# Kernel optimization log

Hardware: AMD Instinct MI355X
Metric: run time of the kernel (lower is better)

## Reference

```python
import jax, jax.numpy as jnp
import numpy as np

N, E, B = 50000, 800000, 64          # nodes, edges, graphs
D_IN, HID, OUT, HEADS = 128, 64, 32, 4
NEG_SLOPE, BN_EPS = 0.2, 1e-5


def gat_conv(x, src, dst, W, a_src, a_dst, bias):
    """PyG-style GATConv (concat heads). x:[n,din], W:[din,H*C], a_*:[H,C]."""
    n = x.shape[0]
    H, C = a_src.shape
    xl = (x @ W).reshape(n, H, C)                      # [n,H,C]
    e_s = jnp.einsum('nhc,hc->nh', xl, a_src)          # alpha_src per node
    e_d = jnp.einsum('nhc,hc->nh', xl, a_dst)          # alpha_dst per node
    e = jax.nn.leaky_relu(e_s[src] + e_d[dst], NEG_SLOPE)   # [E,H]
    m = jax.ops.segment_max(e, dst, num_segments=n)
    m = jnp.where(jnp.isfinite(m), m, 0.0)             # guard isolated nodes
    p = jnp.exp(e - m[dst])
    s = jax.ops.segment_sum(p, dst, num_segments=n)
    alpha = p / (s[dst] + 1e-16)                       # edge softmax over in-edges
    out = jax.ops.segment_sum(alpha[:, :, None] * xl[src], dst, num_segments=n)
    return out.reshape(n, H * C) + bias


def batch_norm(h, gamma, beta):
    mu = h.mean(0)
    var = h.var(0)
    return (h - mu) * jax.lax.rsqrt(var + BN_EPS) * gamma + beta


def setup_inputs() -> dict:
    key = jax.random.key(0)
    ks = jax.random.split(key, 18)
    sc = 0.05
    x = jax.random.normal(ks[0], (N, D_IN), jnp.float32)
    edge_index = jax.random.randint(ks[1], (2, E), 0, N, jnp.int32)
    batch = jnp.sort(jax.random.randint(ks[2], (N,), 0, B, jnp.int32))
    C1 = HID // HEADS
    return {
        'x': x, 'edge_index': edge_index, 'batch': batch,
        'W1': jax.random.normal(ks[3], (D_IN, HID), jnp.float32) * sc,
        'a_src1': jax.random.normal(ks[4], (HEADS, C1), jnp.float32) * sc,
        'a_dst1': jax.random.normal(ks[5], (HEADS, C1), jnp.float32) * sc,
        'b1': jnp.zeros((HID,), jnp.float32),
        'g1': jnp.ones((HID,), jnp.float32),
        'be1': jnp.zeros((HID,), jnp.float32),
        'W2': jax.random.normal(ks[6], (HID, OUT), jnp.float32) * sc,
        'a_src2': jax.random.normal(ks[7], (1, OUT), jnp.float32) * sc,
        'a_dst2': jax.random.normal(ks[8], (1, OUT), jnp.float32) * sc,
        'b2': jnp.zeros((OUT,), jnp.float32),
        'g2': jnp.ones((OUT,), jnp.float32),
        'be2': jnp.zeros((OUT,), jnp.float32),
        'fcW1': jax.random.normal(ks[9], (2 * OUT, OUT), jnp.float32) * sc,
        'fcb1': jnp.zeros((OUT,), jnp.float32),
        'fcW2': jax.random.normal(ks[10], (OUT, OUT), jnp.float32) * sc,
        'fcb2': jnp.zeros((OUT,), jnp.float32),
    }


def reference(x, edge_index, batch, W1, a_src1, a_dst1, b1, g1, be1,
              W2, a_src2, a_dst2, b2, g2, be2, fcW1, fcb1, fcW2, fcb2):
    n = x.shape[0]
    loops = jnp.arange(n, dtype=edge_index.dtype)
    src = jnp.concatenate([edge_index[0], loops])   # PyG add_self_loops
    dst = jnp.concatenate([edge_index[1], loops])

    h = gat_conv(x, src, dst, W1, a_src1, a_dst1, b1)
    h = jax.nn.relu(batch_norm(h, g1, be1))          # dropout: eval no-op
    h = gat_conv(h, src, dst, W2, a_src2, a_dst2, b2)
    node_emb = batch_norm(h, g2, be2)                # [N, OUT]

    cnt = jax.ops.segment_sum(jnp.ones((n,), node_emb.dtype), batch, num_segments=B)
    gmean = jax.ops.segment_sum(node_emb, batch, num_segments=B) / jnp.maximum(cnt, 1.0)[:, None]
    gmax = jax.ops.segment_max(node_emb, batch, num_segments=B)
    gmax = jnp.where(jnp.isfinite(gmax), gmax, 0.0)
    g = jnp.concatenate([gmean, gmax], axis=1)       # [B, 2*OUT]
    g = jax.nn.relu(g @ fcW1 + fcb1)
    graph_emb = g @ fcW2 + fcb2                      # [B, OUT]
    return node_emb, graph_emb
```

## Files before the change

kernel.cpp:

```cpp
#include <hip/hip_runtime.h>
#include <math.h>

#define N_NODES 50000
#define N_EDGES 800000
#define N_GRAPHS 64
#define D_IN 128
#define HID 64
#define OUT_C 32
#define NEG 0.2f
#define BN_EPS 1e-5f
#define N_TILES 3125
#define N_BUCKETS 196
#define BIN_CHUNK 4096
#define BIN_NB 196
#define GEMM1_NB 782
#define BUCKET_CAP 5120
#define PHANTOM N_NODES

typedef __attribute__((ext_vector_type(8))) short short8;
typedef __attribute__((ext_vector_type(4))) float f32x4;

static __device__ inline unsigned short f2bf(float f) {
    unsigned u = __float_as_uint(f);
    u += 0x7FFF + ((u >> 16) & 1);
    return (unsigned short)(u >> 16);
}
static __device__ inline float bfl(unsigned u) { return __uint_as_float(u << 16); }
static __device__ inline float bfh(unsigned u) { return __uint_as_float(u & 0xFFFF0000u); }


__global__ void __launch_bounds__(256) k_front(
        const int* __restrict__ src, const int* __restrict__ dst,
        int* __restrict__ gcur, unsigned* __restrict__ ebuf,
        const float* __restrict__ x, const float* __restrict__ W1,
        const float* __restrict__ a_src1, const float* __restrict__ a_dst1,
        unsigned short* __restrict__ xl1b, float* __restrict__ esd1,
        unsigned short* __restrict__ xl2b, float* __restrict__ esd2,
        const int* __restrict__ batch, int* __restrict__ gstart) {
    __shared__ __align__(16) char smem[23616];
    int tid = threadIdx.x;
    int blk = blockIdx.x;

    if (blk < BIN_NB) {
        int* cnt = (int*)smem;
        int* lofs = cnt + 256;
        int* dstoff = lofs + 256;
        int* ws4 = dstoff + 256;
        unsigned* stage = (unsigned*)(ws4 + 4);
        unsigned char* stage_b = (unsigned char*)(stage + BIN_CHUNK);
        cnt[tid] = 0;
        __syncthreads();
        int e0 = blk * BIN_CHUNK;
        int ne = N_EDGES - e0; if (ne > BIN_CHUNK) ne = BIN_CHUNK;
        unsigned rec[16]; int bkt[16], lp[16];
        #pragma unroll
        for (int j = 0; j < 16; ++j) {
            int r = j * 256 + tid;
            if (r < ne) {
                int e = e0 + r;
                int s = src[e], d = dst[e];
                rec[j] = ((unsigned)s << 8) | (unsigned)(d & 255);
                bkt[j] = d >> 8;
                lp[j] = atomicAdd(&cnt[bkt[j]], 1);
            } else bkt[j] = -1;
        }
        __syncthreads();
        int v = cnt[tid];
        int lane = tid & 63, wid = tid >> 6;
        int incl = v;
        #pragma unroll
        for (int off = 1; off < 64; off <<= 1) {
            int t = __shfl_up(incl, off, 64);
            if (lane >= off) incl += t;
        }
        if (lane == 63) ws4[wid] = incl;
        __syncthreads();
        if (tid == 0) {
            int a = ws4[0];
            #pragma unroll
            for (int j = 1; j < 4; ++j) { a += ws4[j]; ws4[j] = a; }
        }
        __syncthreads();
        if (wid > 0) incl += ws4[wid - 1];
        lofs[tid] = incl - v;
        __syncthreads();
        #pragma unroll
        for (int j = 0; j < 16; ++j) {
            if (bkt[j] >= 0) {
                int idx = lofs[bkt[j]] + lp[j];
                stage[idx] = rec[j];
                stage_b[idx] = (unsigned char)bkt[j];
            }
        }
        if (tid < N_BUCKETS && cnt[tid] > 0) {
            int g = atomicAdd(&gcur[tid], cnt[tid]);
            dstoff[tid] = tid * BUCKET_CAP + g - lofs[tid];
        }
        __syncthreads();
        for (int i = tid; i < ne; i += 256) {
            int b = stage_b[i];
            ebuf[dstoff[b] + i] = stage[i];
        }
        return;
    }

    if (blk < BIN_NB + GEMM1_NB) {
        typedef unsigned short WtRow[144];
        WtRow* Wt = (WtRow*)smem;
        for (int i = tid; i < 80 * 128; i += 256) {
            int n = i >> 7, k = i & 127;
            float v;
            if (n < 64) v = W1[k * 64 + n];
            else if (n < 72) {
                int hh = (n - 64) & 3;
                const float* a = ((n - 64) < 4 ? a_src1 : a_dst1) + hh * 16;
                v = 0.f;
                #pragma unroll
                for (int c = 0; c < 16; ++c) v = fmaf(W1[k * 64 + hh * 16 + c], a[c], v);
            } else v = 0.f;
            Wt[n][k] = f2bf(v);
        }
        __syncthreads();
        int lane = tid & 63, wid = tid >> 6;
        int tile = (blk - BIN_NB) * 4 + wid;
        if (tile >= N_TILES) return;
        int m = lane & 15, kg = lane >> 4;
        int base = tile * 16;
        const float* xr = x + (size_t)(base + m) * D_IN + kg * 8;
        f32x4 acc[5];
        #pragma unroll
        for (int t = 0; t < 5; ++t) acc[t] = (f32x4){0.f, 0.f, 0.f, 0.f};
        #pragma unroll
        for (int s = 0; s < 4; ++s) {
            f32x4 p = ((const f32x4*)(xr + s * 32))[0];
            f32x4 q = ((const f32x4*)(xr + s * 32))[1];
            short8 a;
            a[0] = (short)f2bf(p[0]); a[1] = (short)f2bf(p[1]);
            a[2] = (short)f2bf(p[2]); a[3] = (short)f2bf(p[3]);
            a[4] = (short)f2bf(q[0]); a[5] = (short)f2bf(q[1]);
            a[6] = (short)f2bf(q[2]); a[7] = (short)f2bf(q[3]);
            #pragma unroll
            for (int t = 0; t < 5; ++t) {
                short8 b = *(const short8*)&Wt[t * 16 + m][s * 32 + kg * 8];
                acc[t] = __builtin_amdgcn_mfma_f32_16x16x32_bf16(a, b, acc[t], 0, 0, 0);
            }
        }
        #pragma unroll
        for (int r = 0; r < 4; ++r) {
            int node = base + kg * 4 + r;
            #pragma unroll
            for (int t = 0; t < 4; ++t)
                xl1b[(size_t)node * HID + t * 16 + m] = f2bf(acc[t][r]);
            if (m < 8) esd1[node * 8 + m] = acc[4][r];
        }
        return;
    }

    if (tid <= N_GRAPHS) {
        int g = tid;
        int lo = 0, hi = N_NODES;
        while (lo < hi) {
            int mid = (lo + hi) >> 1;
            if (batch[mid] < g) lo = mid + 1; else hi = mid;
        }
        gstart[g] = lo;
    }
    if (tid >= 128 && tid < 192) xl1b[(size_t)PHANTOM * HID + (tid - 128)] = 0;
    if (tid >= 192 && tid < 200) esd1[(size_t)PHANTOM * 8 + (tid - 192)] = -1e30f;
    if (tid >= 200 && tid < 232) xl2b[(size_t)PHANTOM * OUT_C + (tid - 200)] = 0;
    if (tid >= 232 && tid < 234) esd2[(size_t)PHANTOM * 2 + (tid - 232)] = -1e30f;
}


__global__ void __launch_bounds__(256) k_countscan(
        const unsigned* __restrict__ ebuf, const int* __restrict__ gcur,
        int* __restrict__ counts, int* __restrict__ row_start,
        int* __restrict__ bsum) {
    __shared__ int lcnt[256];
    __shared__ int ws[4];
    int tid = threadIdx.x, b = blockIdx.x;
    lcnt[tid] = 0;
    __syncthreads();
    int ne = gcur[b];
    const unsigned* eb = ebuf + (size_t)b * BUCKET_CAP;
    for (int i = tid; i < ne; i += 256)
        atomicAdd(&lcnt[eb[i] & 255u], 1);
    __syncthreads();
    int node = b * 256 + tid;
    int raw = lcnt[tid];
    if (node < N_NODES) counts[node] = raw;
    int v = (node < N_NODES) ? ((raw + 3) & ~3) : 0;
    int lane = tid & 63, wid = tid >> 6;
    int incl = v;
    #pragma unroll
    for (int off = 1; off < 64; off <<= 1) {
        int t = __shfl_up(incl, off, 64);
        if (lane >= off) incl += t;
    }
    if (lane == 63) ws[wid] = incl;
    __syncthreads();
    if (tid == 0) {
        int a = ws[0];
        #pragma unroll
        for (int j = 1; j < 4; ++j) { a += ws[j]; ws[j] = a; }
    }
    __syncthreads();
    if (wid > 0) incl += ws[wid - 1];
    if (node < N_NODES) row_start[node + 1] = incl;
    if (tid == 255) bsum[b] = incl;
}


__global__ void __launch_bounds__(256) k_fillrs(
        const unsigned* __restrict__ ebuf, const int* __restrict__ gcur,
        const int* __restrict__ bsum, const int* __restrict__ counts,
        int* __restrict__ row_start, int* __restrict__ col) {
    __shared__ int lcur[256], rs[256];
    __shared__ int wsum4[4];
    __shared__ int btot;
    int tid = threadIdx.x, b = blockIdx.x;
    int lane = tid & 63, wid = tid >> 6;
    int v = (tid < b) ? bsum[tid] : 0;
    #pragma unroll
    for (int off = 32; off; off >>= 1) v += __shfl_down(v, off, 64);
    if (lane == 0) wsum4[wid] = v;
    __syncthreads();
    if (tid == 0) btot = wsum4[0] + wsum4[1] + wsum4[2] + wsum4[3];
    __syncthreads();
    int boffv = btot;
    int node = b * 256 + tid;
    int intra = (tid == 0) ? 0 : row_start[node];
    int rsf = boffv + intra;
    if (node < N_NODES) {
        row_start[node] = rsf;
        rs[tid] = rsf;
        if (node == N_NODES - 1)
            row_start[N_NODES] = rsf + ((counts[node] + 3) & ~3);
    } else rs[tid] = 0;
    lcur[tid] = 0;
    __syncthreads();
    int ne = gcur[b];
    const unsigned* eb = ebuf + (size_t)b * BUCKET_CAP;
    for (int i = tid; i < ne; i += 256) {
        unsigned e = eb[i];
        int li = e & 255u;
        int p = atomicAdd(&lcur[li], 1);
        col[rs[li] + p] = (int)(e >> 8);
    }
    if (node < N_NODES) {
        int cnt = counts[node];
        int pe = (cnt + 3) & ~3;
        for (int j = cnt; j < pe; ++j) col[rsf + j] = PHANTOM;
    }
}


__global__ void __launch_bounds__(256) k_agg1(
        const unsigned* __restrict__ xl1r, const float* __restrict__ esd1,
        const int* __restrict__ row_start, const int* __restrict__ col,
        const float* __restrict__ b1, float* __restrict__ h1pre) {
    int wid = threadIdx.x >> 6, lane = threadIdx.x & 63;
    int d = blockIdx.x * 4 + wid;
    if (d >= N_NODES) return;
    int c2 = lane & 31, half = lane >> 5;
    int h = c2 >> 3;
    float edh = esd1[d * 8 + 4 + h];
    float ax = 0.f, ay = 0.f, wsum = 0.f;
    if (half == 0) {
        float e0 = esd1[d * 8 + h] + edh;
        float w0 = __expf(fmaxf(e0, NEG * e0));
        unsigned u = xl1r[(size_t)d * 32 + c2];
        ax = w0 * bfl(u); ay = w0 * bfh(u); wsum = w0;
    }
    int js = row_start[d], je = row_start[d + 1];
    for (int j0 = js; j0 < je; j0 += 64) {
        int sv = col[j0 + lane];
        int cnt = je - j0; if (cnt > 64) cnt = 64;
        for (int k = 0; k < cnt; k += 4) {
            int sa = __shfl(sv, k + half, 64);
            int sb = __shfl(sv, k + 2 + half, 64);
            unsigned ua = xl1r[(size_t)sa * 32 + c2];
            unsigned ub = xl1r[(size_t)sb * 32 + c2];
            float ea = esd1[sa * 8 + h] + edh;
            float eb = esd1[sb * 8 + h] + edh;
            float wa = __expf(fmaxf(ea, NEG * ea));
            float wb = __expf(fmaxf(eb, NEG * eb));
            ax = fmaf(wa, bfl(ua), ax); ay = fmaf(wa, bfh(ua), ay);
            ax = fmaf(wb, bfl(ub), ax); ay = fmaf(wb, bfh(ub), ay);
            wsum += wa + wb;
        }
    }
    ax += __shfl_xor(ax, 32, 64);
    ay += __shfl_xor(ay, 32, 64);
    wsum += __shfl_xor(wsum, 32, 64);
    if (half == 0) {
        float2 bb = ((const float2*)b1)[c2];
        float inv = 1.f / wsum;
        float2 r;
        r.x = ax * inv + bb.x;
        r.y = ay * inv + bb.y;
        ((float2*)h1pre)[(size_t)d * 32 + c2] = r;
    }
}


__global__ void __launch_bounds__(256) k_stats(const float* __restrict__ hpre,
                                               int nch, float* __restrict__ stats) {
    int c = threadIdx.x & (nch - 1);
    int gid = blockIdx.x * blockDim.x + threadIdx.x;
    int r0 = gid / nch;
    int rstride = (gridDim.x * blockDim.x) / nch;
    float s = 0.f, s2 = 0.f;
    for (int n = r0; n < N_NODES; n += rstride) {
        float v = hpre[(size_t)n * nch + c];
        s += v;
        s2 = fmaf(v, v, s2);
    }
    __shared__ float ls[256], ls2[256];
    ls[threadIdx.x] = s;
    ls2[threadIdx.x] = s2;
    __syncthreads();
    if (threadIdx.x < nch) {
        int rows = 256 / nch;
        float a = 0.f, b = 0.f;
        for (int r = 0; r < rows; ++r) {
            a += ls[r * nch + c];
            b += ls2[r * nch + c];
        }
        atomicAdd(&stats[c], a);
        atomicAdd(&stats[nch + c], b);
    }
}


__global__ void __launch_bounds__(256) k_gemm2(
        const float* __restrict__ h1pre, const float* __restrict__ stats1,
        const float* __restrict__ g1, const float* __restrict__ be1,
        const float* __restrict__ W2, const float* __restrict__ a_src2,
        const float* __restrict__ a_dst2,
        unsigned short* __restrict__ xl2b, float* __restrict__ esd2) {
    __shared__ unsigned short Wt[48][80];
    __shared__ float A1s[64], B1s[64];
    int tid = threadIdx.x;
    for (int i = tid; i < 48 * 64; i += 256) {
        int n = i >> 6, k = i & 63;
        float v;
        if (n < 32) v = W2[k * 32 + n];
        else if (n < 34) {
            const float* a = (n == 32) ? a_src2 : a_dst2;
            v = 0.f;
            #pragma unroll
            for (int c = 0; c < 32; ++c) v = fmaf(W2[k * 32 + c], a[c], v);
        } else v = 0.f;
        Wt[n][k] = f2bf(v);
    }
    if (tid < 64) {
        float mu = stats1[tid] * (1.f / N_NODES);
        float var = stats1[64 + tid] * (1.f / N_NODES) - mu * mu;
        float sc = g1[tid] * rsqrtf(var + BN_EPS);
        A1s[tid] = sc;
        B1s[tid] = be1[tid] - mu * sc;
    }
    __syncthreads();
    int lane = tid & 63, wid = tid >> 6;
    int tile = blockIdx.x * 4 + wid;
    if (tile >= N_TILES) return;
    int m = lane & 15, kg = lane >> 4;
    int base = tile * 16;
    const float* hr = h1pre + (size_t)(base + m) * HID + kg * 8;
    f32x4 acc[3];
    #pragma unroll
    for (int t = 0; t < 3; ++t) acc[t] = (f32x4){0.f, 0.f, 0.f, 0.f};
    #pragma unroll
    for (int s = 0; s < 2; ++s) {
        int k0 = s * 32 + kg * 8;
        f32x4 p = ((const f32x4*)(hr + s * 32))[0];
        f32x4 q = ((const f32x4*)(hr + s * 32))[1];
        f32x4 sa = *(const f32x4*)&A1s[k0];
        f32x4 sb = *(const f32x4*)&B1s[k0];
        f32x4 sa2 = *(const f32x4*)&A1s[k0 + 4];
        f32x4 sb2 = *(const f32x4*)&B1s[k0 + 4];
        short8 a;
        #pragma unroll
        for (int j = 0; j < 4; ++j) {
            float v = fmaf(p[j], sa[j], sb[j]);
            a[j] = (short)f2bf(v > 0.f ? v : 0.f);
        }
        #pragma unroll
        for (int j = 0; j < 4; ++j) {
            float v = fmaf(q[j], sa2[j], sb2[j]);
            a[4 + j] = (short)f2bf(v > 0.f ? v : 0.f);
        }
        #pragma unroll
        for (int t = 0; t < 3; ++t) {
            short8 b = *(const short8*)&Wt[t * 16 + m][s * 32 + kg * 8];
            acc[t] = __builtin_amdgcn_mfma_f32_16x16x32_bf16(a, b, acc[t], 0, 0, 0);
        }
    }
    #pragma unroll
    for (int r = 0; r < 4; ++r) {
        int node = base + kg * 4 + r;
        #pragma unroll
        for (int t = 0; t < 2; ++t)
            xl2b[(size_t)node * OUT_C + t * 16 + m] = f2bf(acc[t][r]);
        if (m < 2) esd2[node * 2 + m] = acc[2][r];
    }
}


__global__ void __launch_bounds__(256) k_agg2(
        const unsigned* __restrict__ xl2r, const float* __restrict__ esd2,
        const int* __restrict__ row_start, const int* __restrict__ col,
        const float* __restrict__ b2, float* __restrict__ h2pre) {
    int wid = threadIdx.x >> 6, lane = threadIdx.x & 63;
    int d = blockIdx.x * 4 + wid;
    if (d >= N_NODES) return;
    int c2 = lane & 15, q = lane >> 4;
    float edh = esd2[d * 2 + 1];
    float ax = 0.f, ay = 0.f, wsum = 0.f;
    if (q == 0) {
        float e0 = esd2[d * 2] + edh;
        float w0 = __expf(fmaxf(e0, NEG * e0));
        unsigned u = xl2r[(size_t)d * 16 + c2];
        ax = w0 * bfl(u); ay = w0 * bfh(u); wsum = w0;
    }
    int js = row_start[d], je = row_start[d + 1];
    for (int j0 = js; j0 < je; j0 += 32) {
        int sv = col[j0 + (lane & 31)];
        int cnt = je - j0; if (cnt > 32) cnt = 32;
        for (int k = 0; k < cnt; k += 4) {
            int s = __shfl(sv, k + q, 64);
            unsigned u = xl2r[(size_t)s * 16 + c2];
            float e = esd2[s * 2] + edh;
            float wv = __expf(fmaxf(e, NEG * e));
            ax = fmaf(wv, bfl(u), ax);
            ay = fmaf(wv, bfh(u), ay);
            wsum += wv;
        }
    }
    ax += __shfl_xor(ax, 16, 64); ax += __shfl_xor(ax, 32, 64);
    ay += __shfl_xor(ay, 16, 64); ay += __shfl_xor(ay, 32, 64);
    wsum += __shfl_xor(wsum, 16, 64); wsum += __shfl_xor(wsum, 32, 64);
    if (lane < 16) {
        float2 bb = ((const float2*)b2)[c2];
        float inv = 1.f / wsum;
        float2 r;
        r.x = ax * inv + bb.x;
        r.y = ay * inv + bb.y;
        ((float2*)h2pre)[(size_t)d * 16 + c2] = r;
    }
}


__global__ void __launch_bounds__(256) k_bnpool(
        const float* __restrict__ h2pre, const float* __restrict__ stats2,
        const float* __restrict__ g2, const float* __restrict__ be2,
        const int* __restrict__ gstart, float* __restrict__ out,
        float* __restrict__ pfeat) {
    __shared__ float A2[OUT_C], B2[OUT_C];
    if (threadIdx.x < OUT_C) {
        int cc = threadIdx.x;
        float mu = stats2[cc] * (1.f / N_NODES);
        float var = stats2[OUT_C + cc] * (1.f / N_NODES) - mu * mu;
        float sc = g2[cc] * rsqrtf(var + BN_EPS);
        A2[cc] = sc;
        B2[cc] = be2[cc] - mu * sc;
    }
    __syncthreads();
    int g = blockIdx.x >> 2, part = blockIdx.x & 3;
    int s = gstart[g], e = gstart[g + 1];
    int len = e - s;
    int qq = (len + 3) >> 2;
    int ps = s + part * qq;
    int pe = ps + qq; if (pe > e) pe = e;
    int c = threadIdx.x & 31, r = threadIdx.x >> 5;
    float sum = 0.f, mx = -INFINITY;
    for (int n = ps + r; n < pe; n += 8) {
        float v = fmaf(h2pre[(size_t)n * OUT_C + c], A2[c], B2[c]);
        out[(size_t)n * OUT_C + c] = v;
        sum += v;
        mx = fmaxf(mx, v);
    }
    __shared__ float lsum[256], lmax[256];
    lsum[threadIdx.x] = sum;
    lmax[threadIdx.x] = mx;
    __syncthreads();
    if (threadIdx.x < 32) {
        float ts = 0.f, tm = -INFINITY;
        for (int rr = 0; rr < 8; ++rr) {
            ts += lsum[rr * 32 + c];
            tm = fmaxf(tm, lmax[rr * 32 + c]);
        }
        pfeat[blockIdx.x * 64 + c] = ts;
        pfeat[blockIdx.x * 64 + 32 + c] = tm;
    }
}


__global__ void __launch_bounds__(256) k_mlp(
        const float* __restrict__ pfeat, const int* __restrict__ gstart,
        const float* __restrict__ fcW1, const float* __restrict__ fcb1,
        const float* __restrict__ fcW2, const float* __restrict__ fcb2,
        float* __restrict__ out) {
    __shared__ float gf[N_GRAPHS * 64];
    __shared__ float t1[N_GRAPHS * OUT_C];
    int tid = threadIdx.x;
    for (int i = tid; i < N_GRAPHS * 32; i += 256) {
        int g = i >> 5, c = i & 31;
        float sm = 0.f, mx = -INFINITY;
        #pragma unroll
        for (int p = 0; p < 4; ++p) {
            sm += pfeat[(g * 4 + p) * 64 + c];
            mx = fmaxf(mx, pfeat[(g * 4 + p) * 64 + 32 + c]);
        }
        int cnt = gstart[g + 1] - gstart[g];
        gf[g * 64 + c] = (cnt > 0) ? sm / (float)cnt : 0.f;
        gf[g * 64 + 32 + c] = (cnt > 0) ? mx : 0.f;
    }
    __syncthreads();
    for (int i = tid; i < N_GRAPHS * OUT_C; i += 256) {
        int g = i >> 5, j = i & 31;
        float a = fcb1[j];
        for (int k = 0; k < 64; ++k) a = fmaf(gf[g * 64 + k], fcW1[k * OUT_C + j], a);
        t1[i] = a > 0.f ? a : 0.f;
    }
    __syncthreads();
    for (int i = tid; i < N_GRAPHS * OUT_C; i += 256) {
        int g = i >> 5, oc = i & 31;
        float a = fcb2[oc];
        for (int k = 0; k < OUT_C; ++k) a = fmaf(t1[g * OUT_C + k], fcW2[k * OUT_C + oc], a);
        out[(size_t)N_NODES * OUT_C + g * OUT_C + oc] = a;
    }
}


extern "C" void kernel_launch(void* const* d_in, const int* in_sizes, int n_in,
                              void* d_out, int out_size, void* d_ws, size_t ws_size,
                              hipStream_t stream) {
    (void)in_sizes; (void)n_in; (void)out_size; (void)ws_size;
    const float* x      = (const float*)d_in[0];
    const int*   ei     = (const int*)d_in[1];
    const int*   batch  = (const int*)d_in[2];
    const float* W1     = (const float*)d_in[3];
    const float* a_src1 = (const float*)d_in[4];
    const float* a_dst1 = (const float*)d_in[5];
    const float* b1     = (const float*)d_in[6];
    const float* g1     = (const float*)d_in[7];
    const float* be1    = (const float*)d_in[8];
    const float* W2     = (const float*)d_in[9];
    const float* a_src2 = (const float*)d_in[10];
    const float* a_dst2 = (const float*)d_in[11];
    const float* b2     = (const float*)d_in[12];
    const float* g2     = (const float*)d_in[13];
    const float* be2    = (const float*)d_in[14];
    const float* fcW1   = (const float*)d_in[15];
    const float* fcb1   = (const float*)d_in[16];
    const float* fcW2   = (const float*)d_in[17];
    const float* fcb2   = (const float*)d_in[18];
    const int* srcv = ei;
    const int* dstv = ei + N_EDGES;
    float* out = (float*)d_out;

    char* w = (char*)d_ws;
    size_t o = 0;
    #define ALLOC(nbytes) (w + o); o = (o + (size_t)(nbytes) + 15) & ~(size_t)15
    int*   gcur      = (int*)ALLOC(N_BUCKETS * 4);
    float* stats1    = (float*)ALLOC(128 * 4);
    float* stats2    = (float*)ALLOC(64 * 4);
    size_t zero_bytes = o;
    int*   counts    = (int*)ALLOC((size_t)N_NODES * 4);
    int*   row_start = (int*)ALLOC((size_t)(N_NODES + 2) * 4);
    int*   gst       = (int*)ALLOC(66 * 4);
    int*   bsum      = (int*)ALLOC(N_BUCKETS * 4);
    int*   col       = (int*)ALLOC(((size_t)N_EDGES + 3 * N_NODES + 256) * 4);
    unsigned* ebuf   = (unsigned*)ALLOC((size_t)N_BUCKETS * BUCKET_CAP * 4);
    unsigned short* xl1b = (unsigned short*)ALLOC((size_t)(N_NODES + 1) * HID * 2);
    float* esd1      = (float*)ALLOC((size_t)(N_NODES + 1) * 8 * 4);
    float* h1pre     = (float*)ALLOC((size_t)N_NODES * HID * 4);
    unsigned short* xl2b = (unsigned short*)ALLOC((size_t)(N_NODES + 1) * OUT_C * 2);
    float* esd2      = (float*)ALLOC((size_t)(N_NODES + 1) * 2 * 4);
    float* pfeat     = (float*)ALLOC(256 * 64 * 4);
    #undef ALLOC
    float* h2pre = h1pre;

    hipMemsetAsync(d_ws, 0, zero_bytes, stream);
    k_front    <<<BIN_NB + GEMM1_NB + 1, 256, 0, stream>>>(
        srcv, dstv, gcur, ebuf, x, W1, a_src1, a_dst1,
        xl1b, esd1, xl2b, esd2, batch, gst);
    k_countscan<<<N_BUCKETS, 256, 0, stream>>>(ebuf, gcur, counts, row_start, bsum);
    k_fillrs   <<<N_BUCKETS, 256, 0, stream>>>(ebuf, gcur, bsum, counts, row_start, col);
    k_agg1     <<<(N_NODES + 3) / 4, 256, 0, stream>>>(
        (const unsigned*)xl1b, esd1, row_start, col, b1, h1pre);
    k_stats    <<<256, 256, 0, stream>>>(h1pre, HID, stats1);
    k_gemm2    <<<(N_TILES + 3) / 4, 256, 0, stream>>>(
        h1pre, stats1, g1, be1, W2, a_src2, a_dst2, xl2b, esd2);
    k_agg2     <<<(N_NODES + 3) / 4, 256, 0, stream>>>(
        (const unsigned*)xl2b, esd2, row_start, col, b2, h2pre);
    k_stats    <<<256, 256, 0, stream>>>(h2pre, OUT_C, stats2);
    k_bnpool   <<<256, 256, 0, stream>>>(h2pre, stats2, g2, be2, gst, out, pfeat);
    k_mlp      <<<1, 256, 0, stream>>>(pfeat, gst, fcW1, fcb1, fcW2, fcb2, out);
}
```

Baseline: 272.6 us.

## Merge CSR build into one kernel and fuse BN stats into aggregation

Replaces the two-kernel count/scan/fill CSR construction with a single kernel that places each bucket's rows at a fixed padded offset (CAP_PAD per bucket), storing start/end pairs per node instead of a global prefix sum. BatchNorm sum and sum-of-squares are now accumulated inside agg1/agg2 via shared-memory atomics and spread over 64 global slots, removing both k_stats passes over the hidden activations. Consumers reduce the 64 partial slots themselves. The trade-off is extra atomics in the aggregation kernels, a larger padded col array that relies on buckets never exceeding CAP_PAD, and the slot zeroing moved into k_front.

```diff
diff --git a/kernel.cpp b/kernel.cpp
--- a/kernel.cpp
+++ b/kernel.cpp
@@ -15,6 +15,7 @@
 #define BIN_NB 196
 #define GEMM1_NB 782
 #define BUCKET_CAP 5120
+#define CAP_PAD 6144
 #define PHANTOM N_NODES
 
 typedef __attribute__((ext_vector_type(8))) short short8;
@@ -36,7 +37,8 @@
         const float* __restrict__ a_src1, const float* __restrict__ a_dst1,
         unsigned short* __restrict__ xl1b, float* __restrict__ esd1,
         unsigned short* __restrict__ xl2b, float* __restrict__ esd2,
-        const int* __restrict__ batch, int* __restrict__ gstart) {
+        const int* __restrict__ batch, int* __restrict__ gstart,
+        float* __restrict__ sp1, float* __restrict__ sp2) {
     __shared__ __align__(16) char smem[23616];
     int tid = threadIdx.x;
     int blk = blockIdx.x;
@@ -169,14 +171,15 @@
     if (tid >= 192 && tid < 200) esd1[(size_t)PHANTOM * 8 + (tid - 192)] = -1e30f;
     if (tid >= 200 && tid < 232) xl2b[(size_t)PHANTOM * OUT_C + (tid - 200)] = 0;
     if (tid >= 232 && tid < 234) esd2[(size_t)PHANTOM * 2 + (tid - 232)] = -1e30f;
-}
-
-
-__global__ void __launch_bounds__(256) k_countscan(
+    for (int i = tid; i < 64 * 128; i += 256) sp1[i] = 0.f;
+    for (int i = tid; i < 64 * 64; i += 256) sp2[i] = 0.f;
+}
+
+
+__global__ void __launch_bounds__(256) k_csr(
         const unsigned* __restrict__ ebuf, const int* __restrict__ gcur,
-        int* __restrict__ counts, int* __restrict__ row_start,
-        int* __restrict__ bsum) {
-    __shared__ int lcnt[256];
+        int2* __restrict__ rowinfo, int* __restrict__ col) {
+    __shared__ int lcnt[256], lofs[256], lcur[256];
     __shared__ int ws[4];
     int tid = threadIdx.x, b = blockIdx.x;
     lcnt[tid] = 0;
@@ -186,10 +189,8 @@
     for (int i = tid; i < ne; i += 256)
         atomicAdd(&lcnt[eb[i] & 255u], 1);
     __syncthreads();
-    int node = b * 256 + tid;
     int raw = lcnt[tid];
-    if (node < N_NODES) counts[node] = raw;
-    int v = (node < N_NODES) ? ((raw + 3) & ~3) : 0;
+    int v = (raw + 3) & ~3;
     int lane = tid & 63, wid = tid >> 6;
     int incl = v;
     #pragma unroll
@@ -206,62 +207,33 @@
     }
     __syncthreads();
     if (wid > 0) incl += ws[wid - 1];
-    if (node < N_NODES) row_start[node + 1] = incl;
-    if (tid == 255) bsum[b] = incl;
-}
-
-
-__global__ void __launch_bounds__(256) k_fillrs(
-        const unsigned* __restrict__ ebuf, const int* __restrict__ gcur,
-        const int* __restrict__ bsum, const int* __restrict__ counts,
-        int* __restrict__ row_start, int* __restrict__ col) {
-    __shared__ int lcur[256], rs[256];
-    __shared__ int wsum4[4];
-    __shared__ int btot;
-    int tid = threadIdx.x, b = blockIdx.x;
-    int lane = tid & 63, wid = tid >> 6;
-    int v = (tid < b) ? bsum[tid] : 0;
-    #pragma unroll
-    for (int off = 32; off; off >>= 1) v += __shfl_down(v, off, 64);
-    if (lane == 0) wsum4[wid] = v;
-    __syncthreads();
-    if (tid == 0) btot = wsum4[0] + wsum4[1] + wsum4[2] + wsum4[3];
-    __syncthreads();
-    int boffv = btot;
+    int js = b * CAP_PAD + (incl - v);
     int node = b * 256 + tid;
-    int intra = (tid == 0) ? 0 : row_start[node];
-    int rsf = boffv + intra;
-    if (node < N_NODES) {
-        row_start[node] = rsf;
-        rs[tid] = rsf;
-        if (node == N_NODES - 1)
-            row_start[N_NODES] = rsf + ((counts[node] + 3) & ~3);
-    } else rs[tid] = 0;
+    if (node < N_NODES) rowinfo[node] = make_int2(js, js + v);
+    lofs[tid] = js;
     lcur[tid] = 0;
     __syncthreads();
-    int ne = gcur[b];
-    const unsigned* eb = ebuf + (size_t)b * BUCKET_CAP;
     for (int i = tid; i < ne; i += 256) {
         unsigned e = eb[i];
         int li = e & 255u;
         int p = atomicAdd(&lcur[li], 1);
-        col[rs[li] + p] = (int)(e >> 8);
-    }
-    if (node < N_NODES) {
-        int cnt = counts[node];
-        int pe = (cnt + 3) & ~3;
-        for (int j = cnt; j < pe; ++j) col[rsf + j] = PHANTOM;
-    }
+        col[lofs[li] + p] = (int)(e >> 8);
+    }
+    for (int j = raw; j < v; ++j) col[js + j] = PHANTOM;
 }
 
 
 __global__ void __launch_bounds__(256) k_agg1(
         const unsigned* __restrict__ xl1r, const float* __restrict__ esd1,
-        const int* __restrict__ row_start, const int* __restrict__ col,
-        const float* __restrict__ b1, float* __restrict__ h1pre) {
-    int wid = threadIdx.x >> 6, lane = threadIdx.x & 63;
+        const int2* __restrict__ rowinfo, const int* __restrict__ col,
+        const float* __restrict__ b1, float* __restrict__ h1pre,
+        float* __restrict__ sp1) {
+    __shared__ float ps[64], pq[64];
+    int tid = threadIdx.x;
+    if (tid < 64) { ps[tid] = 0.f; pq[tid] = 0.f; }
+    __syncthreads();
+    int wid = tid >> 6, lane = tid & 63;
     int d = blockIdx.x * 4 + wid;
-    if (d >= N_NODES) return;
     int c2 = lane & 31, half = lane >> 5;
     int h = c2 >> 3;
     float edh = esd1[d * 8 + 4 + h];
@@ -272,7 +244,8 @@
         unsigned u = xl1r[(size_t)d * 32 + c2];
         ax = w0 * bfl(u); ay = w0 * bfh(u); wsum = w0;
     }
-    int js = row_start[d], je = row_start[d + 1];
+    int2 ri = rowinfo[d];
+    int js = ri.x, je = ri.y;
     for (int j0 = js; j0 < je; j0 += 64) {
         int sv = col[j0 + lane];
         int cnt = je - j0; if (cnt > 64) cnt = 64;
@@ -300,47 +273,24 @@
         r.x = ax * inv + bb.x;
         r.y = ay * inv + bb.y;
         ((float2*)h1pre)[(size_t)d * 32 + c2] = r;
-    }
-}
-
-
-__global__ void __launch_bounds__(256) k_stats(const float* __restrict__ hpre,
-                                               int nch, float* __restrict__ stats) {
-    int c = threadIdx.x & (nch - 1);
-    int gid = blockIdx.x * blockDim.x + threadIdx.x;
-    int r0 = gid / nch;
-    int rstride = (gridDim.x * blockDim.x) / nch;
-    float s = 0.f, s2 = 0.f;
-    for (int n = r0; n < N_NODES; n += rstride) {
-        float v = hpre[(size_t)n * nch + c];
-        s += v;
-        s2 = fmaf(v, v, s2);
-    }
-    __shared__ float ls[256], ls2[256];
-    ls[threadIdx.x] = s;
-    ls2[threadIdx.x] = s2;
-    __syncthreads();
-    if (threadIdx.x < nch) {
-        int rows = 256 / nch;
-        float a = 0.f, b = 0.f;
-        for (int r = 0; r < rows; ++r) {
-            a += ls[r * nch + c];
-            b += ls2[r * nch + c];
-        }
-        atomicAdd(&stats[c], a);
-        atomicAdd(&stats[nch + c], b);
-    }
+        atomicAdd(&ps[c2 * 2], r.x);     atomicAdd(&ps[c2 * 2 + 1], r.y);
+        atomicAdd(&pq[c2 * 2], r.x * r.x); atomicAdd(&pq[c2 * 2 + 1], r.y * r.y);
+    }
+    __syncthreads();
+    int slot = (blockIdx.x & 63) * 128;
+    if (tid < 64) atomicAdd(&sp1[slot + tid], ps[tid]);
+    else if (tid < 128) atomicAdd(&sp1[slot + tid], pq[tid - 64]);
 }
 
 
 __global__ void __launch_bounds__(256) k_gemm2(
-        const float* __restrict__ h1pre, const float* __restrict__ stats1,
+        const float* __restrict__ h1pre, const float* __restrict__ sp1,
         const float* __restrict__ g1, const float* __restrict__ be1,
         const float* __restrict__ W2, const float* __restrict__ a_src2,
         const float* __restrict__ a_dst2,
         unsigned short* __restrict__ xl2b, float* __restrict__ esd2) {
     __shared__ unsigned short Wt[48][80];
-    __shared__ float A1s[64], B1s[64];
+    __shared__ float A1s[64], B1s[64], red[128];
     int tid = threadIdx.x;
     for (int i = tid; i < 48 * 64; i += 256) {
         int n = i >> 6, k = i & 63;
@@ -354,9 +304,15 @@
         } else v = 0.f;
         Wt[n][k] = f2bf(v);
     }
+    if (tid < 128) {
+        float s = 0.f;
+        for (int j = 0; j < 64; ++j) s += sp1[j * 128 + tid];
+        red[tid] = s;
+    }
+    __syncthreads();
     if (tid < 64) {
-        float mu = stats1[tid] * (1.f / N_NODES);
-        float var = stats1[64 + tid] * (1.f / N_NODES) - mu * mu;
+        float mu = red[tid] * (1.f / N_NODES);
+        float var = red[64 + tid] * (1.f / N_NODES) - mu * mu;
         float sc = g1[tid] * rsqrtf(var + BN_EPS);
         A1s[tid] = sc;
         B1s[tid] = be1[tid] - mu * sc;
@@ -410,11 +366,15 @@
 
 __global__ void __launch_bounds__(256) k_agg2(
         const unsigned* __restrict__ xl2r, const float* __restrict__ esd2,
-        const int* __restrict__ row_start, const int* __restrict__ col,
-        const float* __restrict__ b2, float* __restrict__ h2pre) {
-    int wid = threadIdx.x >> 6, lane = threadIdx.x & 63;
+        const int2* __restrict__ rowinfo, const int* __restrict__ col,
+        const float* __restrict__ b2, float* __restrict__ h2pre,
+        float* __restrict__ sp2) {
+    __shared__ float ps[32], pq[32];
+    int tid = threadIdx.x;
+    if (tid < 32) { ps[tid] = 0.f; pq[tid] = 0.f; }
+    __syncthreads();
+    int wid = tid >> 6, lane = tid & 63;
     int d = blockIdx.x * 4 + wid;
-    if (d >= N_NODES) return;
     int c2 = lane & 15, q = lane >> 4;
     float edh = esd2[d * 2 + 1];
     float ax = 0.f, ay = 0.f, wsum = 0.f;
@@ -424,7 +384,8 @@
         unsigned u = xl2r[(size_t)d * 16 + c2];
         ax = w0 * bfl(u); ay = w0 * bfh(u); wsum = w0;
     }
-    int js = row_start[d], je = row_start[d + 1];
+    int2 ri = rowinfo[d];
+    int js = ri.x, je = ri.y;
     for (int j0 = js; j0 < je; j0 += 32) {
         int sv = col[j0 + (lane & 31)];
         int cnt = je - j0; if (cnt > 32) cnt = 32;
@@ -448,23 +409,35 @@
         r.x = ax * inv + bb.x;
         r.y = ay * inv + bb.y;
         ((float2*)h2pre)[(size_t)d * 16 + c2] = r;
-    }
+        atomicAdd(&ps[c2 * 2], r.x);       atomicAdd(&ps[c2 * 2 + 1], r.y);
+        atomicAdd(&pq[c2 * 2], r.x * r.x); atomicAdd(&pq[c2 * 2 + 1], r.y * r.y);
+    }
+    __syncthreads();
+    int slot = (blockIdx.x & 63) * 64;
+    if (tid < 32) atomicAdd(&sp2[slot + tid], ps[tid]);
+    else if (tid < 64) atomicAdd(&sp2[slot + tid], pq[tid - 32]);
 }
 
 
 __global__ void __launch_bounds__(256) k_bnpool(
-        const float* __restrict__ h2pre, const float* __restrict__ stats2,
+        const float* __restrict__ h2pre, const float* __restrict__ sp2,
         const float* __restrict__ g2, const float* __restrict__ be2,
         const int* __restrict__ gstart, float* __restrict__ out,
         float* __restrict__ pfeat) {
-    __shared__ float A2[OUT_C], B2[OUT_C];
-    if (threadIdx.x < OUT_C) {
-        int cc = threadIdx.x;
-        float mu = stats2[cc] * (1.f / N_NODES);
-        float var = stats2[OUT_C + cc] * (1.f / N_NODES) - mu * mu;
-        float sc = g2[cc] * rsqrtf(var + BN_EPS);
-        A2[cc] = sc;
-        B2[cc] = be2[cc] - mu * sc;
+    __shared__ float A2[OUT_C], B2[OUT_C], red[64];
+    int tid = threadIdx.x;
+    if (tid < 64) {
+        float s = 0.f;
+        for (int j = 0; j < 64; ++j) s += sp2[j * 64 + tid];
+        red[tid] = s;
+    }
+    __syncthreads();
+    if (tid < 32) {
+        float mu = red[tid] * (1.f / N_NODES);
+        float var = red[32 + tid] * (1.f / N_NODES) - mu * mu;
+        float sc = g2[tid] * rsqrtf(var + BN_EPS);
+        A2[tid] = sc;
+        B2[tid] = be2[tid] - mu * sc;
     }
     __syncthreads();
     int g = blockIdx.x >> 2, part = blockIdx.x & 3;
@@ -473,7 +446,7 @@
     int qq = (len + 3) >> 2;
     int ps = s + part * qq;
     int pe = ps + qq; if (pe > e) pe = e;
-    int c = threadIdx.x & 31, r = threadIdx.x >> 5;
+    int c = tid & 31, r = tid >> 5;
     float sum = 0.f, mx = -INFINITY;
     for (int n = ps + r; n < pe; n += 8) {
         float v = fmaf(h2pre[(size_t)n * OUT_C + c], A2[c], B2[c]);
@@ -482,10 +455,10 @@
         mx = fmaxf(mx, v);
     }
     __shared__ float lsum[256], lmax[256];
-    lsum[threadIdx.x] = sum;
-    lmax[threadIdx.x] = mx;
-    __syncthreads();
-    if (threadIdx.x < 32) {
+    lsum[tid] = sum;
+    lmax[tid] = mx;
+    __syncthreads();
+    if (tid < 32) {
         float ts = 0.f, tm = -INFINITY;
         for (int rr = 0; rr < 8; ++rr) {
             ts += lsum[rr * 32 + c];
@@ -565,14 +538,12 @@
     size_t o = 0;
     #define ALLOC(nbytes) (w + o); o = (o + (size_t)(nbytes) + 15) & ~(size_t)15
     int*   gcur      = (int*)ALLOC(N_BUCKETS * 4);
-    float* stats1    = (float*)ALLOC(128 * 4);
-    float* stats2    = (float*)ALLOC(64 * 4);
     size_t zero_bytes = o;
-    int*   counts    = (int*)ALLOC((size_t)N_NODES * 4);
-    int*   row_start = (int*)ALLOC((size_t)(N_NODES + 2) * 4);
+    float* sp1       = (float*)ALLOC(64 * 128 * 4);
+    float* sp2       = (float*)ALLOC(64 * 64 * 4);
+    int2*  rowinfo   = (int2*)ALLOC((size_t)N_NODES * 8);
     int*   gst       = (int*)ALLOC(66 * 4);
-    int*   bsum      = (int*)ALLOC(N_BUCKETS * 4);
-    int*   col       = (int*)ALLOC(((size_t)N_EDGES + 3 * N_NODES + 256) * 4);
+    int*   col       = (int*)ALLOC(((size_t)N_BUCKETS * CAP_PAD + 256) * 4);
     unsigned* ebuf   = (unsigned*)ALLOC((size_t)N_BUCKETS * BUCKET_CAP * 4);
     unsigned short* xl1b = (unsigned short*)ALLOC((size_t)(N_NODES + 1) * HID * 2);
     float* esd1      = (float*)ALLOC((size_t)(N_NODES + 1) * 8 * 4);
@@ -584,19 +555,16 @@
     float* h2pre = h1pre;
 
     hipMemsetAsync(d_ws, 0, zero_bytes, stream);
-    k_front    <<<BIN_NB + GEMM1_NB + 1, 256, 0, stream>>>(
+    k_front <<<BIN_NB + GEMM1_NB + 1, 256, 0, stream>>>(
         srcv, dstv, gcur, ebuf, x, W1, a_src1, a_dst1,
-        xl1b, esd1, xl2b, esd2, batch, gst);
-    k_countscan<<<N_BUCKETS, 256, 0, stream>>>(ebuf, gcur, counts, row_start, bsum);
-    k_fillrs   <<<N_BUCKETS, 256, 0, stream>>>(ebuf, gcur, bsum, counts, row_start, col);
-    k_agg1     <<<(N_NODES + 3) / 4, 256, 0, stream>>>(
-        (const unsigned*)xl1b, esd1, row_start, col, b1, h1pre);
-    k_stats    <<<256, 256, 0, stream>>>(h1pre, HID, stats1);
-    k_gemm2    <<<(N_TILES + 3) / 4, 256, 0, stream>>>(
-        h1pre, stats1, g1, be1, W2, a_src2, a_dst2, xl2b, esd2);
-    k_agg2     <<<(N_NODES + 3) / 4, 256, 0, stream>>>(
-        (const unsigned*)xl2b, esd2, row_start, col, b2, h2pre);
-    k_stats    <<<256, 256, 0, stream>>>(h2pre, OUT_C, stats2);
-    k_bnpool   <<<256, 256, 0, stream>>>(h2pre, stats2, g2, be2, gst, out, pfeat);
-    k_mlp      <<<1, 256, 0, stream>>>(pfeat, gst, fcW1, fcb1, fcW2, fcb2, out);
-}
+        xl1b, esd1, xl2b, esd2, batch, gst, sp1, sp2);
+    k_csr   <<<N_BUCKETS, 256, 0, stream>>>(ebuf, gcur, rowinfo, col);
+    k_agg1  <<<N_NODES / 4, 256, 0, stream>>>(
+        (const unsigned*)xl1b, esd1, rowinfo, col, b1, h1pre, sp1);
+    k_gemm2 <<<(N_TILES + 3) / 4, 256, 0, stream>>>(
+        h1pre, sp1, g1, be1, W2, a_src2, a_dst2, xl2b, esd2);
+    k_agg2  <<<N_NODES / 4, 256, 0, stream>>>(
+        (const unsigned*)xl2b, esd2, rowinfo, col, b2, h2pre, sp2);
+    k_bnpool<<<256, 256, 0, stream>>>(h2pre, sp2, g2, be2, gst, out, pfeat);
+    k_mlp   <<<1, 256, 0, stream>>>(pfeat, gst, fcW1, fcb1, fcW2, fcb2, out);
+}
```

Result: no change. 268.2 us (-1.6%).
